# Optimization experiments

Measured on AMD Instinct MI355X. Metric: run time of the kernel, lower is better.

## Reference

```python
import jax, jax.numpy as jnp
import numpy as np

B, Z, D, H, L = 65536, 14, 32, 64, 7  # batch, z_dim, trace_dim, hidden_dim, n_colonies/lines

# Standard 0-indexed Fano lines (i, j, k)
FANO = np.array([[0, 1, 2], [0, 3, 4], [0, 5, 6], [1, 3, 5], [1, 4, 6], [2, 3, 6], [2, 4, 5]])
SRC = jnp.asarray(FANO[:, [0, 1, 2]])  # source colony per ordered pair   [7,3]
PAR = jnp.asarray(FANO[:, [1, 2, 0]])  # partner colony per ordered pair  [7,3]
GATE_THRESHOLD = 0.3

# Catastrophe-specific activations per colony (spark..crystal order)
ACTS = [jax.nn.relu, jnp.tanh, lambda x: jax.nn.gelu(x, approximate=False), jax.nn.silu,
        jax.nn.softplus, jax.nn.sigmoid, lambda x: jnp.clip(x, -1.0, 1.0)]


def _ln(x, g, b):
    m = x.mean(-1, keepdims=True)
    v = ((x - m) ** 2).mean(-1, keepdims=True)
    return (x - m) / jnp.sqrt(v + 1e-5) * g + b


def _l2norm(x):
    # matches F.normalize(dim=-1) with eps=1e-12
    n = jnp.linalg.norm(x, axis=-1, keepdims=True)
    return x / jnp.maximum(n, 1e-12)


def setup_inputs() -> dict:
    key = jax.random.key(0)
    ks = iter(jax.random.split(key, 16))

    def p(shape, s=0.1):
        return jax.random.normal(next(ks), shape, dtype=jnp.float32) * s

    return {
        "z": jax.random.normal(next(ks), (B, L, Z), dtype=jnp.float32),
        # per-colony trace generator: Linear(Z,H) -> LN -> act -> Linear(H,D)
        "gen_W1": p((L, Z, H)), "gen_b1": jnp.zeros((L, H), jnp.float32),
        "gen_g": jnp.ones((L, H), jnp.float32), "gen_be": jnp.zeros((L, H), jnp.float32),
        "gen_W2": p((L, H, D)), "gen_b2": jnp.zeros((L, D), jnp.float32),
        # per-colony confidence head: Linear(Z,H//2) -> ReLU -> Linear(H//2,1) -> Sigmoid
        "cf_W1": p((L, Z, H // 2)), "cf_b1": jnp.zeros((L, H // 2), jnp.float32),
        "cf_W2": p((L, H // 2, 1)), "cf_b2": jnp.zeros((L, 1), jnp.float32),
        # line gate: Linear(7*D, 7) -> Sigmoid
        "g_W": p((L * D, L)), "g_b": jnp.zeros((L,), jnp.float32),
        # 7 line composers: Linear(2D,H) -> LN -> ReLU -> Linear(H,D)
        "c_W1": p((L, 2 * D, H)), "c_b1": jnp.zeros((L, H), jnp.float32),
        "c_g": jnp.ones((L, H), jnp.float32), "c_be": jnp.zeros((L, H), jnp.float32),
        "c_W2": p((L, H, D)), "c_b2": jnp.zeros((L, D), jnp.float32),
    }


def _forward(z, gen_W1, gen_b1, gen_g, gen_be, gen_W2, gen_b2,
             cf_W1, cf_b1, cf_W2, cf_b2, g_W, g_b,
             c_W1, c_b1, c_g, c_be, c_W2, c_b2):
    # --- ColonyTraceGenerator (vectorized over batch, colony-specific activation) ---
    h = jnp.einsum("bcz,czh->bch", z, gen_W1) + gen_b1          # [B,7,H]
    h = _ln(h, gen_g, gen_be)
    a = jnp.stack([ACTS[c](h[:, c]) for c in range(L)], axis=1)  # fixed 7-colony loop
    traces = jnp.einsum("bch,chd->bcd", a, gen_W2) + gen_b2      # [B,7,D]
    traces = _l2norm(traces)

    hc = jax.nn.relu(jnp.einsum("bcz,czh->bch", z, cf_W1) + cf_b1)
    conf = jax.nn.sigmoid((jnp.einsum("bch,cho->bco", hc, cf_W2) + cf_b2)[..., 0])  # [B,7]

    # --- FanoTracePropagator ---
    gates = jax.nn.sigmoid(traces.reshape(B, L * D) @ g_W + g_b)  # [B,7]

    # ordered pairs per line: (i,j)->k, (j,k)->i, (k,i)->j
    pair_in = jnp.concatenate([traces[:, SRC], traces[:, PAR]], axis=-1)      # [B,7,3,2D]
    ch = jnp.einsum("blpi,lih->blph", pair_in, c_W1) + c_b1[:, None]           # [B,7,3,H]
    ch = jax.nn.relu(_ln(ch, c_g[:, None], c_be[:, None]))
    cv = jnp.einsum("blph,lhd->blpd", ch, c_W2) + c_b2[:, None]                # [B,7,3,D]
    cv = gates[:, :, None, None] * _l2norm(cv)

    # original skips lines with gate < 0.3 -> zero them out in the batched form
    active = gates >= GATE_THRESHOLD                                           # [B,7]
    composed = jnp.where(active[:, :, None, None], cv, 0.0)                    # [B,7,3,D]
    comp_conf = jnp.where(active[:, :, None],
                          conf[:, SRC] * conf[:, PAR] * gates[:, :, None], 0.0)  # [B,7,3]
    return composed, comp_conf


def reference(z, gen_W1, gen_b1, gen_g, gen_be, gen_W2, gen_b2,
              cf_W1, cf_b1, cf_W2, cf_b2, g_W, g_b,
              c_W1, c_b1, c_g, c_be, c_W2, c_b2):
    return _forward(z, gen_W1, gen_b1, gen_g, gen_be, gen_W2, gen_b2,
                    cf_W1, cf_b1, cf_W2, cf_b2, g_W, g_b,
                    c_W1, c_b1, c_g, c_be, c_W2, c_b2)
```

## Files before the change

kernel.cpp:

```cpp
#include <hip/hip_runtime.h>
#include <math.h>

#define NB 65536

typedef short s16x8 __attribute__((ext_vector_type(8)));
typedef float f32x4 __attribute__((ext_vector_type(4)));

#define SZ_TR     ((size_t)7*NB*32*2)
#define OFF_TRHI  ((size_t)0)
#define OFF_TRLO  (OFF_TRHI + SZ_TR)
#define OFF_CONF  (OFF_TRLO + SZ_TR)
#define SZ_CONF   ((size_t)7*NB*4)
#define OFF_PART  (OFF_CONF + SZ_CONF)
#define SZ_PART   ((size_t)49*NB*4)
#define OFF_GATE  (OFF_PART + SZ_PART)
#define SZ_GATE   ((size_t)7*NB*4)
#define OFF_W1H   (OFF_GATE + SZ_GATE)
#define SZ_W1F    ((size_t)7*4*2*64*16)
#define OFF_W1L   (OFF_W1H + SZ_W1F)
#define OFF_W2H   (OFF_W1L + SZ_W1F)
#define SZ_W2F    ((size_t)7*2*2*64*16)
#define OFF_W2L   (OFF_W2H + SZ_W2F)
#define OFF_G2H   (OFF_W2L + SZ_W2F)
#define SZ_G2     ((size_t)7*2*2*64*16)
#define OFF_G2L   (OFF_G2H + SZ_G2)

static __device__ const int T_SRC[21] = {0,1,2, 0,3,4, 0,5,6, 1,3,5, 1,4,6, 2,3,6, 2,4,5};
static __device__ const int T_PAR[21] = {1,2,0, 3,4,0, 5,6,0, 3,5,1, 4,6,1, 3,6,2, 4,5,2};

__device__ __forceinline__ float sigf(float x) { return 1.f / (1.f + expf(-x)); }

__device__ __forceinline__ unsigned bfrnd(float x) {
    unsigned u = __builtin_bit_cast(unsigned, x);
    return (u + 0x7FFFu + ((u >> 16) & 1u)) >> 16;
}
__device__ __forceinline__ float bfval(unsigned h) {
    return __builtin_bit_cast(float, h << 16);
}

__device__ __forceinline__ f32x4 mfma16(s16x8 a, s16x8 b, f32x4 c) {
    return __builtin_amdgcn_mfma_f32_16x16x32_bf16(a, b, c, 0, 0, 0);
}

__device__ __forceinline__ void pack8(const float* v, s16x8& hi, s16x8& lo) {
    uint4 hu, lu;
    unsigned h[8], l[8];
    #pragma unroll
    for (int i = 0; i < 8; ++i) {
        h[i] = bfrnd(v[i]);
        float rem = v[i] - bfval(h[i]);
        l[i] = bfrnd(rem);
    }
    hu.x = h[0] | (h[1] << 16); hu.y = h[2] | (h[3] << 16);
    hu.z = h[4] | (h[5] << 16); hu.w = h[6] | (h[7] << 16);
    lu.x = l[0] | (l[1] << 16); lu.y = l[2] | (l[3] << 16);
    lu.z = l[4] | (l[5] << 16); lu.w = l[6] | (l[7] << 16);
    hi = __builtin_bit_cast(s16x8, hu);
    lo = __builtin_bit_cast(s16x8, lu);
}

__global__ __launch_bounds__(256, 4)
void colP(const float* __restrict__ c_W1, const float* __restrict__ c_W2,
          const float* __restrict__ gen_W2,
          uint4* __restrict__ w1h, uint4* __restrict__ w1l,
          uint4* __restrict__ w2h, uint4* __restrict__ w2l,
          uint4* __restrict__ g2h, uint4* __restrict__ g2l)
{
    const int e = blockIdx.x * 256 + threadIdx.x;
    if (e < 3584) {
        const int lane = e & 63, er = e >> 6;
        const int ks = er & 1, mt = (er >> 1) & 3, l = er >> 3;
        const int j  = mt * 16 + (lane & 15);
        const int k0 = ks * 32 + (lane >> 4) * 8;
        float v[8];
        #pragma unroll
        for (int jj = 0; jj < 8; ++jj) v[jj] = c_W1[((size_t)(l * 64 + k0 + jj)) * 64 + j];
        s16x8 hi, lo; pack8(v, hi, lo);
        w1h[e] = __builtin_bit_cast(uint4, hi);
        w1l[e] = __builtin_bit_cast(uint4, lo);
    } else if (e < 5376) {
        const int e2 = e - 3584;
        const int lane = e2 & 63, er = e2 >> 6;
        const int ks2 = er & 1, mt2 = (er >> 1) & 1, l = er >> 2;
        const int d  = mt2 * 16 + (lane & 15);
        const int k0 = ks2 * 32 + (lane >> 4) * 8;
        float v[8];
        #pragma unroll
        for (int jj = 0; jj < 8; ++jj) v[jj] = c_W2[((size_t)(l * 64 + k0 + jj)) * 32 + d];
        s16x8 hi, lo; pack8(v, hi, lo);
        w2h[e2] = __builtin_bit_cast(uint4, hi);
        w2l[e2] = __builtin_bit_cast(uint4, lo);
    } else if (e < 7168) {
        const int e2 = e - 5376;
        const int lane = e2 & 63, er = e2 >> 6;
        const int ks2 = er & 1, mt2 = (er >> 1) & 1, c = er >> 2;
        const int d  = mt2 * 16 + (lane & 15);
        const int k0 = ks2 * 32 + (lane >> 4) * 8;
        float v[8];
        #pragma unroll
        for (int jj = 0; jj < 8; ++jj) v[jj] = gen_W2[((size_t)(c * 64 + k0 + jj)) * 32 + d];
        s16x8 hi, lo; pack8(v, hi, lo);
        g2h[e2] = __builtin_bit_cast(uint4, hi);
        g2l[e2] = __builtin_bit_cast(uint4, lo);
    }
}

__global__ __launch_bounds__(256) __attribute__((amdgpu_waves_per_eu(4, 4)))
void colA1(const float* __restrict__ z,
           const float* __restrict__ gen_W1, const float* __restrict__ gen_b1,
           const float* __restrict__ gen_g,  const float* __restrict__ gen_be,
           const float* __restrict__ cf_W1,  const float* __restrict__ cf_b1,
           const float* __restrict__ cf_W2,  const float* __restrict__ cf_b2,
           uint4* __restrict__ actHI, uint4* __restrict__ actLO,
           float* __restrict__ conf)
{
    const int c = blockIdx.x >> 8;
    const int b = ((blockIdx.x & 255) << 8) + threadIdx.x;

    float zv[14];
    {
        const float* zp = z + ((size_t)b * 7 + (size_t)c) * 14;
        #pragma unroll
        for (int i = 0; i < 7; ++i) {
            float2 u = *(const float2*)(zp + 2 * i);
            zv[2*i] = u.x; zv[2*i+1] = u.y;
        }
    }

    {
        float hc[32];
        const float* bp = cf_b1 + c * 32;
        #pragma unroll
        for (int k = 0; k < 32; ++k) hc[k] = bp[k];
        const float* W = cf_W1 + c * 14 * 32;
        for (int i = 0; i < 14; ++i) {
            const float zi = zv[i];
            const float* w = W + i * 32;
            #pragma unroll
            for (int k = 0; k < 32; ++k) hc[k] = fmaf(zi, w[k], hc[k]);
        }
        float cl = cf_b2[c];
        const float* w2 = cf_W2 + c * 32;
        #pragma unroll
        for (int k = 0; k < 32; ++k) cl = fmaf(fmaxf(hc[k], 0.f), w2[k], cl);
        conf[(size_t)c * NB + b] = sigf(cl);
    }

    float h[64];
    {
        const float* bp = gen_b1 + c * 64;
        #pragma unroll
        for (int j = 0; j < 64; ++j) h[j] = bp[j];
        const float* W = gen_W1 + c * 14 * 64;
        for (int i = 0; i < 14; ++i) {
            const float zi = zv[i];
            const float* w = W + i * 64;
            #pragma unroll
            for (int j = 0; j < 64; ++j) h[j] = fmaf(zi, w[j], h[j]);
        }
    }
    {
        float m = 0.f;
        #pragma unroll
        for (int j = 0; j < 64; ++j) m += h[j];
        m *= (1.f / 64.f);
        float v = 0.f;
        #pragma unroll
        for (int j = 0; j < 64; ++j) { float d = h[j] - m; v = fmaf(d, d, v); }
        v *= (1.f / 64.f);
        const float rs = 1.f / sqrtf(v + 1e-5f);
        const float* gp = gen_g  + c * 64;
        const float* bp = gen_be + c * 64;
        #pragma unroll
        for (int j = 0; j < 64; ++j) h[j] = (h[j] - m) * rs * gp[j] + bp[j];
    }
    switch (c) {
        case 0:
            #pragma unroll
            for (int j = 0; j < 64; ++j) h[j] = fmaxf(h[j], 0.f);
            break;
        case 1:
            #pragma unroll
            for (int j = 0; j < 64; ++j) h[j] = tanhf(h[j]);
            break;
        case 2:
            #pragma unroll
            for (int j = 0; j < 64; ++j) h[j] = 0.5f * h[j] * (1.f + erff(h[j] * 0.70710678118654752f));
            break;
        case 3:
            #pragma unroll
            for (int j = 0; j < 64; ++j) h[j] = h[j] * sigf(h[j]);
            break;
        case 4:
            #pragma unroll
            for (int j = 0; j < 64; ++j) h[j] = fmaxf(h[j], 0.f) + log1pf(expf(-fabsf(h[j])));
            break;
        case 5:
            #pragma unroll
            for (int j = 0; j < 64; ++j) h[j] = sigf(h[j]);
            break;
        default:
            #pragma unroll
            for (int j = 0; j < 64; ++j) h[j] = fminf(fmaxf(h[j], -1.f), 1.f);
            break;
    }
    {
        const size_t abase = ((size_t)c * NB + b) * 8;
        #pragma unroll
        for (int k = 0; k < 8; ++k) {
            unsigned hw[4], lw[4];
            #pragma unroll
            for (int i = 0; i < 4; ++i) {
                const int e = 8 * k + 2 * i;
                unsigned h0 = bfrnd(h[e]), h1 = bfrnd(h[e+1]);
                float r0 = h[e]   - bfval(h0);
                float r1 = h[e+1] - bfval(h1);
                hw[i] = h0 | (h1 << 16);
                lw[i] = bfrnd(r0) | (bfrnd(r1) << 16);
            }
            uint4 u; u.x = hw[0]; u.y = hw[1]; u.z = hw[2]; u.w = hw[3];
            actHI[abase + k] = u;
            uint4 v; v.x = lw[0]; v.y = lw[1]; v.z = lw[2]; v.w = lw[3];
            actLO[abase + k] = v;
        }
    }
}

__global__ __launch_bounds__(256, 4)
void colA2(const uint4* __restrict__ actHI, const uint4* __restrict__ actLO,
           const uint4* __restrict__ g2h, const uint4* __restrict__ g2l,
           const float* __restrict__ gen_b2,
           float* __restrict__ tn_ws)
{
    const int wave = threadIdx.x >> 6;
    const int lane = threadIdx.x & 63;
    const int q    = lane >> 4;
    const int bl   = lane & 15;
    const int c    = blockIdx.x >> 6;
    const int base = ((blockIdx.x & 63) << 10) + (wave << 8);

    s16x8 a2h[2][2], a2l[2][2];
    #pragma unroll
    for (int mt = 0; mt < 2; ++mt)
        #pragma unroll
        for (int ks = 0; ks < 2; ++ks) {
            a2h[mt][ks] = __builtin_bit_cast(s16x8, g2h[((c * 2 + mt) * 2 + ks) * 64 + lane]);
            a2l[mt][ks] = __builtin_bit_cast(s16x8, g2l[((c * 2 + mt) * 2 + ks) * 64 + lane]);
        }
    f32x4 b2v[2];
    {
        const f32x4* p2 = (const f32x4*)(gen_b2 + (size_t)c * 32);
        #pragma unroll
        for (int mt = 0; mt < 2; ++mt) b2v[mt] = p2[4 * mt + q];
    }

    for (int it = 0; it < 16; ++it) {
        const int bg = base + it * 16 + bl;
        const size_t ab = ((size_t)c * NB + bg) * 8;

        s16x8 bh0 = __builtin_bit_cast(s16x8, actHI[ab + q]);
        s16x8 bl0 = __builtin_bit_cast(s16x8, actLO[ab + q]);
        s16x8 bh1 = __builtin_bit_cast(s16x8, actHI[ab + 4 + q]);
        s16x8 bl1 = __builtin_bit_cast(s16x8, actLO[ab + 4 + q]);

        f32x4 d0 = {0.f,0.f,0.f,0.f}, d1 = {0.f,0.f,0.f,0.f};
        d0 = mfma16(a2h[0][0], bh0, d0);
        d0 = mfma16(a2h[0][0], bl0, d0);
        d0 = mfma16(a2l[0][0], bh0, d0);
        d1 = mfma16(a2h[1][0], bh0, d1);
        d1 = mfma16(a2h[1][0], bl0, d1);
        d1 = mfma16(a2l[1][0], bh0, d1);
        d0 = mfma16(a2h[0][1], bh1, d0);
        d0 = mfma16(a2h[0][1], bl1, d0);
        d0 = mfma16(a2l[0][1], bh1, d0);
        d1 = mfma16(a2h[1][1], bh1, d1);
        d1 = mfma16(a2h[1][1], bl1, d1);
        d1 = mfma16(a2l[1][1], bh1, d1);

        d0 += b2v[0];
        d1 += b2v[1];

        float ss = 0.f;
        #pragma unroll
        for (int r = 0; r < 4; ++r) { ss = fmaf(d0[r], d0[r], ss); ss = fmaf(d1[r], d1[r], ss); }
        ss += __shfl_xor(ss, 16);
        ss += __shfl_xor(ss, 32);
        const float inv = 1.f / fmaxf(sqrtf(ss), 1e-12f);

        #pragma unroll
        for (int r = 0; r < 4; ++r)
            tn_ws[((size_t)(c * 32 + 4 * q + r)) * NB + bg] = d0[r] * inv;
        #pragma unroll
        for (int r = 0; r < 4; ++r)
            tn_ws[((size_t)(c * 32 + 16 + 4 * q + r)) * NB + bg] = d1[r] * inv;
    }
}

__global__ __launch_bounds__(256, 4)
void colB1(const float* __restrict__ tn_ws, const float* __restrict__ g_W,
           uint4* __restrict__ trHI, uint4* __restrict__ trLO,
           float* __restrict__ part)
{
    const int c = blockIdx.x >> 8;
    const int b = ((blockIdx.x & 255) << 8) + threadIdx.x;

    float tn[32];
    #pragma unroll
    for (int d = 0; d < 32; ++d) tn[d] = tn_ws[((size_t)(c * 32 + d)) * NB + b];

    {
        const size_t base = ((size_t)c * NB + b) * 4;
        #pragma unroll
        for (int k = 0; k < 4; ++k) {
            unsigned hw[4], lw[4];
            #pragma unroll
            for (int i = 0; i < 4; ++i) {
                const int e = 8 * k + 2 * i;
                unsigned h0 = bfrnd(tn[e]),   h1 = bfrnd(tn[e+1]);
                float r0 = tn[e]   - bfval(h0);
                float r1 = tn[e+1] - bfval(h1);
                hw[i] = h0 | (h1 << 16);
                lw[i] = bfrnd(r0) | (bfrnd(r1) << 16);
            }
            uint4 u; u.x = hw[0]; u.y = hw[1]; u.z = hw[2]; u.w = hw[3];
            trHI[base + k] = u;
            uint4 v; v.x = lw[0]; v.y = lw[1]; v.z = lw[2]; v.w = lw[3];
            trLO[base + k] = v;
        }
    }
    {
        float p[7] = {0.f,0.f,0.f,0.f,0.f,0.f,0.f};
        for (int k = 0; k < 32; ++k) {
            const float v = tn[k];
            const float* w = g_W + (c * 32 + k) * 7;
            #pragma unroll
            for (int l2 = 0; l2 < 7; ++l2) p[l2] = fmaf(v, w[l2], p[l2]);
        }
        #pragma unroll
        for (int l2 = 0; l2 < 7; ++l2) part[((size_t)(c * 7 + l2)) * NB + b] = p[l2];
    }
}

__global__ __launch_bounds__(256, 4)
void colB2(const float* __restrict__ g_b,
           const float* __restrict__ part, const float* __restrict__ conf,
           float* __restrict__ gates, float* __restrict__ out2)
{
    const int b = blockIdx.x * 256 + threadIdx.x;

    float g[7];
    #pragma unroll
    for (int l = 0; l < 7; ++l) g[l] = g_b[l];
    for (int c = 0; c < 7; ++c) {
        #pragma unroll
        for (int l = 0; l < 7; ++l) g[l] += part[((size_t)(c * 7 + l)) * NB + b];
    }
    #pragma unroll
    for (int l = 0; l < 7; ++l) {
        g[l] = sigf(g[l]);
        gates[(size_t)l * NB + b] = g[l];
    }

    float cf[7];
    #pragma unroll
    for (int c = 0; c < 7; ++c) cf[c] = conf[(size_t)c * NB + b];

    float* op = out2 + (size_t)b * 21;
    #pragma unroll
    for (int t = 0; t < 21; ++t) {
        const int l = t / 3;
        const float gl = g[l];
        op[t] = (gl >= 0.3f) ? cf[T_SRC[t]] * cf[T_PAR[t]] * gl : 0.f;
    }
}

__global__ __launch_bounds__(256, 2)
void colC(const uint4* __restrict__ trHI, const uint4* __restrict__ trLO,
          const float* __restrict__ gates,
          const uint4* __restrict__ w1fh, const uint4* __restrict__ w1fl,
          const uint4* __restrict__ w2fh, const uint4* __restrict__ w2fl,
          const float* __restrict__ c_b1,
          const float* __restrict__ c_g,  const float* __restrict__ c_be,
          const float* __restrict__ c_b2, float* __restrict__ out)
{
    __shared__ float lds[4][16 * 68];

    const int wave = threadIdx.x >> 6;
    const int lane = threadIdx.x & 63;
    const int q    = lane >> 4;
    const int bl   = lane & 15;

    const int t   = blockIdx.x >> 6;
    const int l   = t / 3;
    const int src = T_SRC[t];
    const int par = T_PAR[t];
    const int base = ((blockIdx.x & 63) << 10) + (wave << 8);

    s16x8 w1h[4][2], w1l[4][2], w2h[2][2], w2l[2][2];
    #pragma unroll
    for (int mt = 0; mt < 4; ++mt)
        #pragma unroll
        for (int ks = 0; ks < 2; ++ks) {
            w1h[mt][ks] = __builtin_bit_cast(s16x8, w1fh[((l * 4 + mt) * 2 + ks) * 64 + lane]);
            w1l[mt][ks] = __builtin_bit_cast(s16x8, w1fl[((l * 4 + mt) * 2 + ks) * 64 + lane]);
        }
    #pragma unroll
    for (int mt = 0; mt < 2; ++mt)
        #pragma unroll
        for (int ks = 0; ks < 2; ++ks) {
            w2h[mt][ks] = __builtin_bit_cast(s16x8, w2fh[((l * 2 + mt) * 2 + ks) * 64 + lane]);
            w2l[mt][ks] = __builtin_bit_cast(s16x8, w2fl[((l * 2 + mt) * 2 + ks) * 64 + lane]);
        }

    f32x4 b1v[4], gv[4], bev[4], b2v[2];
    {
        const f32x4* p1 = (const f32x4*)(c_b1 + (size_t)l * 64);
        const f32x4* pg = (const f32x4*)(c_g  + (size_t)l * 64);
        const f32x4* pb = (const f32x4*)(c_be + (size_t)l * 64);
        #pragma unroll
        for (int mt = 0; mt < 4; ++mt) {
            b1v[mt] = p1[4 * mt + q]; gv[mt] = pg[4 * mt + q]; bev[mt] = pb[4 * mt + q];
        }
        const f32x4* p2 = (const f32x4*)(c_b2 + (size_t)l * 32);
        #pragma unroll
        for (int mt = 0; mt < 2; ++mt) b2v[mt] = p2[4 * mt + q];
    }

    float* ldsw = &lds[wave][0];

    for (int it = 0; it < 16; ++it) {
        const int bg = base + it * 16 + bl;

        const size_t sb = ((size_t)src * NB + bg) * 4 + q;
        const size_t pb = ((size_t)par * NB + bg) * 4 + q;
        s16x8 bsh = __builtin_bit_cast(s16x8, trHI[sb]);
        s16x8 bsl = __builtin_bit_cast(s16x8, trLO[sb]);
        s16x8 bph = __builtin_bit_cast(s16x8, trHI[pb]);
        s16x8 bpl = __builtin_bit_cast(s16x8, trLO[pb]);
        const float gate = gates[(size_t)l * NB + bg];

        f32x4 acc[4];
        #pragma unroll
        for (int mt = 0; mt < 4; ++mt) {
            f32x4 a = {0.f, 0.f, 0.f, 0.f};
            a = mfma16(w1h[mt][0], bsh, a);
            a = mfma16(w1h[mt][0], bsl, a);
            a = mfma16(w1l[mt][0], bsh, a);
            a = mfma16(w1h[mt][1], bph, a);
            a = mfma16(w1h[mt][1], bpl, a);
            a = mfma16(w1l[mt][1], bph, a);
            acc[mt] = a;
        }
        #pragma unroll
        for (int mt = 0; mt < 4; ++mt) acc[mt] += b1v[mt];

        float s = 0.f;
        #pragma unroll
        for (int mt = 0; mt < 4; ++mt)
            #pragma unroll
            for (int r = 0; r < 4; ++r) s += acc[mt][r];
        s += __shfl_xor(s, 16);
        s += __shfl_xor(s, 32);
        const float mean = s * (1.f / 64.f);
        float v = 0.f;
        #pragma unroll
        for (int mt = 0; mt < 4; ++mt)
            #pragma unroll
            for (int r = 0; r < 4; ++r) { float d = acc[mt][r] - mean; v = fmaf(d, d, v); }
        v += __shfl_xor(v, 16);
        v += __shfl_xor(v, 32);
        const float rs = 1.f / sqrtf(v * (1.f / 64.f) + 1e-5f);

        #pragma unroll
        for (int mt = 0; mt < 4; ++mt) {
            f32x4 x;
            #pragma unroll
            for (int r = 0; r < 4; ++r)
                x[r] = fmaxf(fmaf((acc[mt][r] - mean) * rs, gv[mt][r], bev[mt][r]), 0.f);
            *(f32x4*)&ldsw[bl * 68 + 16 * mt + 4 * q] = x;
        }

        f32x4 d0 = {0.f,0.f,0.f,0.f}, d1 = {0.f,0.f,0.f,0.f};
        #pragma unroll
        for (int ks2 = 0; ks2 < 2; ++ks2) {
            f32x4 c0 = *(const f32x4*)&ldsw[bl * 68 + 32 * ks2 + 8 * q];
            f32x4 c1 = *(const f32x4*)&ldsw[bl * 68 + 32 * ks2 + 8 * q + 4];
            float vv[8] = {c0[0], c0[1], c0[2], c0[3], c1[0], c1[1], c1[2], c1[3]};
            s16x8 chh, chl; pack8(vv, chh, chl);
            d0 = mfma16(w2h[0][ks2], chh, d0);
            d0 = mfma16(w2h[0][ks2], chl, d0);
            d0 = mfma16(w2l[0][ks2], chh, d0);
            d1 = mfma16(w2h[1][ks2], chh, d1);
            d1 = mfma16(w2h[1][ks2], chl, d1);
            d1 = mfma16(w2l[1][ks2], chh, d1);
        }
        d0 += b2v[0];
        d1 += b2v[1];

        float ss = 0.f;
        #pragma unroll
        for (int r = 0; r < 4; ++r) { ss = fmaf(d0[r], d0[r], ss); ss = fmaf(d1[r], d1[r], ss); }
        ss += __shfl_xor(ss, 16);
        ss += __shfl_xor(ss, 32);
        const float inv   = 1.f / fmaxf(sqrtf(ss), 1e-12f);
        const float scale = (gate >= 0.3f) ? gate * inv : 0.f;

        float* op = out + (size_t)bg * 672 + t * 32;
        f32x4 o0, o1;
        #pragma unroll
        for (int r = 0; r < 4; ++r) { o0[r] = d0[r] * scale; o1[r] = d1[r] * scale; }
        *(f32x4*)(op + 4 * q)      = o0;
        *(f32x4*)(op + 16 + 4 * q) = o1;
    }
}

extern "C" void kernel_launch(void* const* d_in, const int* in_sizes, int n_in,
                              void* d_out, int out_size, void* d_ws, size_t ws_size,
                              hipStream_t stream) {
    const float* z      = (const float*)d_in[0];
    const float* gen_W1 = (const float*)d_in[1];
    const float* gen_b1 = (const float*)d_in[2];
    const float* gen_g  = (const float*)d_in[3];
    const float* gen_be = (const float*)d_in[4];
    const float* gen_W2 = (const float*)d_in[5];
    const float* gen_b2 = (const float*)d_in[6];
    const float* cf_W1  = (const float*)d_in[7];
    const float* cf_b1  = (const float*)d_in[8];
    const float* cf_W2  = (const float*)d_in[9];
    const float* cf_b2  = (const float*)d_in[10];
    const float* g_W    = (const float*)d_in[11];
    const float* g_b    = (const float*)d_in[12];
    const float* c_W1   = (const float*)d_in[13];
    const float* c_b1   = (const float*)d_in[14];
    const float* c_g    = (const float*)d_in[15];
    const float* c_be   = (const float*)d_in[16];
    const float* c_W2   = (const float*)d_in[17];
    const float* c_b2   = (const float*)d_in[18];

    char* wsb = (char*)d_ws;
    uint4* trHI  = (uint4*)(wsb + OFF_TRHI);
    uint4* trLO  = (uint4*)(wsb + OFF_TRLO);
    float* conf  = (float*)(wsb + OFF_CONF);
    float* part  = (float*)(wsb + OFF_PART);
    float* gates = (float*)(wsb + OFF_GATE);
    uint4* w1fh  = (uint4*)(wsb + OFF_W1H);
    uint4* w1fl  = (uint4*)(wsb + OFF_W1L);
    uint4* w2fh  = (uint4*)(wsb + OFF_W2H);
    uint4* w2fl  = (uint4*)(wsb + OFF_W2L);
    uint4* g2h   = (uint4*)(wsb + OFF_G2H);
    uint4* g2l   = (uint4*)(wsb + OFF_G2L);

    float* outp = (float*)d_out;
    float* out2 = outp + (size_t)NB * 672;

    uint4* actHI = (uint4*)outp;
    uint4* actLO = actHI + (size_t)7 * NB * 8;
    float* tn_ws = outp + (size_t)29360128;

    colP<<<dim3(28), dim3(256), 0, stream>>>(
        c_W1, c_W2, gen_W2, w1fh, w1fl, w2fh, w2fl, g2h, g2l);
    colA1<<<dim3(7 * 256), dim3(256), 0, stream>>>(
        z, gen_W1, gen_b1, gen_g, gen_be, cf_W1, cf_b1, cf_W2, cf_b2,
        actHI, actLO, conf);
    colA2<<<dim3(7 * 64), dim3(256), 0, stream>>>(
        actHI, actLO, g2h, g2l, gen_b2, tn_ws);
    colB1<<<dim3(7 * 256), dim3(256), 0, stream>>>(
        tn_ws, g_W, trHI, trLO, part);
    colB2<<<dim3(256), dim3(256), 0, stream>>>(g_b, part, conf, gates, out2);
    colC<<<dim3(21 * 64), dim3(256), 0, stream>>>(
        trHI, trLO, gates, w1fh, w1fl, w2fh, w2fl,
        c_b1, c_g, c_be, c_b2, outp);
}
```

Baseline: 523.3 us.

## Recompute gen hidden layer in 16-wide chunks to cut register pressure in colA1

The generator's first layer in colA1 is now computed in 16-column chunks. A first pass accumulates only the sum and sum of squares for LayerNorm, and a second pass recomputes each chunk to apply normalization, activation and hi/lo bf16 packing. This replaces the 64-float hidden array held in registers, and the variance now uses the one-pass E[x^2]-mean^2 form. The aim is lower VGPR use and therefore more resident waves, at the cost of doing the 14x64 FMA matmul twice and a small numeric change in the variance.

```diff
diff --git a/kernel.cpp b/kernel.cpp
--- a/kernel.cpp
+++ b/kernel.cpp
@@ -59,6 +59,40 @@
     lo = __builtin_bit_cast(s16x8, lu);
 }
 
+template <int N>
+__device__ __forceinline__ void actN(int c, float* a) {
+    switch (c) {
+        case 0:
+            #pragma unroll
+            for (int u = 0; u < N; ++u) a[u] = fmaxf(a[u], 0.f);
+            break;
+        case 1:
+            #pragma unroll
+            for (int u = 0; u < N; ++u) a[u] = tanhf(a[u]);
+            break;
+        case 2:
+            #pragma unroll
+            for (int u = 0; u < N; ++u) a[u] = 0.5f * a[u] * (1.f + erff(a[u] * 0.70710678118654752f));
+            break;
+        case 3:
+            #pragma unroll
+            for (int u = 0; u < N; ++u) a[u] = a[u] * sigf(a[u]);
+            break;
+        case 4:
+            #pragma unroll
+            for (int u = 0; u < N; ++u) a[u] = fmaxf(a[u], 0.f) + log1pf(expf(-fabsf(a[u])));
+            break;
+        case 5:
+            #pragma unroll
+            for (int u = 0; u < N; ++u) a[u] = sigf(a[u]);
+            break;
+        default:
+            #pragma unroll
+            for (int u = 0; u < N; ++u) a[u] = fminf(fmaxf(a[u], -1.f), 1.f);
+            break;
+    }
+}
+
 __global__ __launch_bounds__(256, 4)
 void colP(const float* __restrict__ c_W1, const float* __restrict__ c_W2,
           const float* __restrict__ gen_W2,
@@ -105,7 +139,7 @@
     }
 }
 
-__global__ __launch_bounds__(256) __attribute__((amdgpu_waves_per_eu(4, 4)))
+__global__ __launch_bounds__(256, 4)
 void colA1(const float* __restrict__ z,
            const float* __restrict__ gen_W1, const float* __restrict__ gen_b1,
            const float* __restrict__ gen_g,  const float* __restrict__ gen_be,
@@ -146,82 +180,69 @@
         conf[(size_t)c * NB + b] = sigf(cl);
     }
 
-    float h[64];
-    {
-        const float* bp = gen_b1 + c * 64;
-        #pragma unroll
-        for (int j = 0; j < 64; ++j) h[j] = bp[j];
-        const float* W = gen_W1 + c * 14 * 64;
+    const float* W1p = gen_W1 + c * 14 * 64;
+    const float* b1p = gen_b1 + c * 64;
+
+    float sum = 0.f, ssq = 0.f;
+    #pragma unroll 1
+    for (int j0 = 0; j0 < 64; j0 += 16) {
+        float hj[16];
+        #pragma unroll
+        for (int u = 0; u < 16; ++u) hj[u] = b1p[j0 + u];
+        #pragma unroll
         for (int i = 0; i < 14; ++i) {
             const float zi = zv[i];
-            const float* w = W + i * 64;
-            #pragma unroll
-            for (int j = 0; j < 64; ++j) h[j] = fmaf(zi, w[j], h[j]);
-        }
-    }
-    {
-        float m = 0.f;
-        #pragma unroll
-        for (int j = 0; j < 64; ++j) m += h[j];
-        m *= (1.f / 64.f);
-        float v = 0.f;
-        #pragma unroll
-        for (int j = 0; j < 64; ++j) { float d = h[j] - m; v = fmaf(d, d, v); }
-        v *= (1.f / 64.f);
-        const float rs = 1.f / sqrtf(v + 1e-5f);
-        const float* gp = gen_g  + c * 64;
-        const float* bp = gen_be + c * 64;
-        #pragma unroll
-        for (int j = 0; j < 64; ++j) h[j] = (h[j] - m) * rs * gp[j] + bp[j];
-    }
-    switch (c) {
-        case 0:
-            #pragma unroll
-            for (int j = 0; j < 64; ++j) h[j] = fmaxf(h[j], 0.f);
-            break;
-        case 1:
-            #pragma unroll
-            for (int j = 0; j < 64; ++j) h[j] = tanhf(h[j]);
-            break;
-        case 2:
-            #pragma unroll
-            for (int j = 0; j < 64; ++j) h[j] = 0.5f * h[j] * (1.f + erff(h[j] * 0.70710678118654752f));
-            break;
-        case 3:
-            #pragma unroll
-            for (int j = 0; j < 64; ++j) h[j] = h[j] * sigf(h[j]);
-            break;
-        case 4:
-            #pragma unroll
-            for (int j = 0; j < 64; ++j) h[j] = fmaxf(h[j], 0.f) + log1pf(expf(-fabsf(h[j])));
-            break;
-        case 5:
-            #pragma unroll
-            for (int j = 0; j < 64; ++j) h[j] = sigf(h[j]);
-            break;
-        default:
-            #pragma unroll
-            for (int j = 0; j < 64; ++j) h[j] = fminf(fmaxf(h[j], -1.f), 1.f);
-            break;
-    }
-    {
+            const float* w = W1p + i * 64 + j0;
+            #pragma unroll
+            for (int u = 0; u < 16; ++u) hj[u] = fmaf(zi, w[u], hj[u]);
+        }
+        #pragma unroll
+        for (int u = 0; u < 16; ++u) { sum += hj[u]; ssq = fmaf(hj[u], hj[u], ssq); }
+    }
+    const float mean = sum * (1.f / 64.f);
+    const float var  = fmaxf(ssq * (1.f / 64.f) - mean * mean, 0.f);
+    const float rs   = 1.f / sqrtf(var + 1e-5f);
+
+    #pragma unroll
+    for (int i = 0; i < 14; ++i) asm volatile("" : "+v"(zv[i]));
+
+    {
+        const float* gp  = gen_g  + c * 64;
+        const float* bep = gen_be + c * 64;
         const size_t abase = ((size_t)c * NB + b) * 8;
-        #pragma unroll
-        for (int k = 0; k < 8; ++k) {
-            unsigned hw[4], lw[4];
-            #pragma unroll
-            for (int i = 0; i < 4; ++i) {
-                const int e = 8 * k + 2 * i;
-                unsigned h0 = bfrnd(h[e]), h1 = bfrnd(h[e+1]);
-                float r0 = h[e]   - bfval(h0);
-                float r1 = h[e+1] - bfval(h1);
-                hw[i] = h0 | (h1 << 16);
-                lw[i] = bfrnd(r0) | (bfrnd(r1) << 16);
+        #pragma unroll 1
+        for (int j0 = 0; j0 < 64; j0 += 16) {
+            float a16[16];
+            #pragma unroll
+            for (int u = 0; u < 16; ++u) a16[u] = b1p[j0 + u];
+            #pragma unroll
+            for (int i = 0; i < 14; ++i) {
+                const float zi = zv[i];
+                const float* w = W1p + i * 64 + j0;
+                #pragma unroll
+                for (int u = 0; u < 16; ++u) a16[u] = fmaf(zi, w[u], a16[u]);
             }
-            uint4 u; u.x = hw[0]; u.y = hw[1]; u.z = hw[2]; u.w = hw[3];
-            actHI[abase + k] = u;
-            uint4 v; v.x = lw[0]; v.y = lw[1]; v.z = lw[2]; v.w = lw[3];
-            actLO[abase + k] = v;
+            #pragma unroll
+            for (int u = 0; u < 16; ++u)
+                a16[u] = fmaf((a16[u] - mean) * rs, gp[j0 + u], bep[j0 + u]);
+            actN<16>(c, a16);
+            #pragma unroll
+            for (int half = 0; half < 2; ++half) {
+                unsigned hw[4], lw[4];
+                #pragma unroll
+                for (int i = 0; i < 4; ++i) {
+                    const int e = half * 8 + 2 * i;
+                    unsigned h0 = bfrnd(a16[e]), h1 = bfrnd(a16[e+1]);
+                    float r0 = a16[e]   - bfval(h0);
+                    float r1 = a16[e+1] - bfval(h1);
+                    hw[i] = h0 | (h1 << 16);
+                    lw[i] = bfrnd(r0) | (bfrnd(r1) << 16);
+                }
+                uint4 u4; u4.x = hw[0]; u4.y = hw[1]; u4.z = hw[2]; u4.w = hw[3];
+                actHI[abase + (j0 >> 3) + half] = u4;
+                uint4 v4; v4.x = lw[0]; v4.y = lw[1]; v4.z = lw[2]; v4.w = lw[3];
+                actLO[abase + (j0 >> 3) + half] = v4;
+            }
         }
     }
 }
```

Result: faster. 485.4 us (-7.2%).
